# Optimization experiments

Measured on AMD Instinct MI355X. Metric: run time of the kernel, lower is better.

The kernel has to match this reference:

```python
import jax, jax.numpy as jnp
import numpy as np

NEG_SLOPE = 0.2  # PyG GATConv default negative_slope
EPS = 1e-16


def gat_conv(x, W, att_src, att_dst, bias, src, dst, heads, out_ch, concat):
    """PyG-style GATConv (eval mode, self-loops already included in src/dst).
    x: [N, F_in]; W: [heads*out_ch, F_in]; att_src/att_dst: [1, heads, out_ch]; bias: [heads*out_ch] or [out_ch].
    """
    N = x.shape[0]
    h = (x @ W.T).reshape(N, heads, out_ch)            # [N, H, C]
    a_src = (h * att_src).sum(-1)                      # [N, H]
    a_dst = (h * att_dst).sum(-1)                      # [N, H]
    alpha = jax.nn.leaky_relu(a_src[src] + a_dst[dst], NEG_SLOPE)  # [E, H]
    # segment softmax over destination nodes
    amax = jax.ops.segment_max(alpha, dst, num_segments=N)         # [N, H]
    ex = jnp.exp(alpha - amax[dst])
    denom = jax.ops.segment_sum(ex, dst, num_segments=N)           # [N, H]
    coef = ex / (denom[dst] + EPS)                                 # [E, H]
    out = jax.ops.segment_sum(h[src] * coef[:, :, None], dst, num_segments=N)  # [N, H, C]
    if concat:
        out = out.reshape(N, heads * out_ch)
    else:
        out = out.mean(axis=1)
    return out + bias


def setup_inputs() -> dict:
    key = jax.random.key(0)
    ks = jax.random.split(key, 10)
    N, F_in, H, C, OUT, E = 50000, 128, 4, 64, 2, 800000
    x = jax.random.normal(ks[0], (N, F_in), dtype=jnp.float32)
    edge_index = jax.random.randint(ks[1], (2, E), 0, N, dtype=jnp.int64)
    glorot = lambda k, shp: jax.random.normal(k, shp, dtype=jnp.float32) * jnp.sqrt(2.0 / (shp[0] + shp[-1]))
    W1 = glorot(ks[2], (H * C, F_in))
    att_src1 = glorot(ks[3], (1, H, C))
    att_dst1 = glorot(ks[4], (1, H, C))
    b1 = jnp.zeros((H * C,), dtype=jnp.float32)
    W2 = glorot(ks[5], (1 * OUT, H * C))
    att_src2 = glorot(ks[6], (1, 1, OUT))
    att_dst2 = glorot(ks[7], (1, 1, OUT))
    b2 = jnp.zeros((OUT,), dtype=jnp.float32)
    return {"x": x, "edge_index": edge_index, "W1": W1, "att_src1": att_src1,
            "att_dst1": att_dst1, "b1": b1, "W2": W2, "att_src2": att_src2,
            "att_dst2": att_dst2, "b2": b2}


def reference(x, edge_index, W1, att_src1, att_dst1, b1, W2, att_src2, att_dst2, b2):
    N = x.shape[0]
    loop = jnp.arange(N, dtype=edge_index.dtype)
    src = jnp.concatenate([edge_index[0], loop])   # add self-loops (PyG default)
    dst = jnp.concatenate([edge_index[1], loop])
    h = gat_conv(x, W1, att_src1, att_dst1, b1, src, dst, heads=4, out_ch=64, concat=True)
    h = jax.nn.relu(h)
    out = gat_conv(h, W2, att_src2, att_dst2, b2, src, dst, heads=1, out_ch=2, concat=False)
    return out
```

## Files before the change

kernel.cpp:

```cpp
#include <hip/hip_runtime.h>
#include <hip/hip_bf16.h>
#include <stdint.h>

#define NEG_SLOPE 0.2f
#define EPSV 1e-16f
#define SLOT 64
#define NBQ 128
#define NBUCKET 391
#define CAPA 32
#define EPB 8192
#define OVCAP 64

typedef __attribute__((ext_vector_type(8))) short bf16x8;
typedef __attribute__((ext_vector_type(4))) float f32x4;

static __device__ __forceinline__ float b2f(unsigned short u) {
    union { float f; uint32_t i; } v; v.i = ((uint32_t)u) << 16; return v.f;
}
static __device__ __forceinline__ uint32_t qpk(float a, float b) {
    union { float f; uint32_t u; } x, y; x.f = a; y.f = b;
    return ((x.u + 0x8000u) >> 16) | ((y.u + 0x8000u) & 0xFFFF0000u);
}

static __device__ __forceinline__ float edge_exp(float as, float ad) {
    float a = as + ad;
    a = a > 0.f ? a : NEG_SLOPE * a;
    return __expf(a);
}

__global__ __launch_bounds__(256) void fused_front_kernel(
    const float* __restrict__ x, const float* __restrict__ W1,
    const float* __restrict__ att_src1, const float* __restrict__ att_dst1,
    const float* __restrict__ b1, const float* __restrict__ W2,
    const int* __restrict__ ei, int E,
    unsigned short* __restrict__ h1,
    float4* __restrict__ a_src1v, float4* __restrict__ a_dst1v,
    unsigned int* __restrict__ bins, unsigned short* __restrict__ counts,
    unsigned int* __restrict__ gov, unsigned int* __restrict__ govcnt,
    float* __restrict__ b1p, float* __restrict__ w2p0, float* __restrict__ w2p1,
    int N, int nblk_gemm, int nblk_binA)
{
    const int b = blockIdx.x, t = threadIdx.x;

    if (b < nblk_gemm) {
        const int wv = t >> 6, lane = t & 63;
        const int l15 = lane & 15, quad = lane >> 4;
        const int m0 = b * 128 + wv * 32;

        union { bf16x8 v; uint32_t u[4]; } A[2][4];
        #pragma unroll
        for (int ms = 0; ms < 2; ++ms) {
            int m = m0 + ms * 16 + l15;
            int mr = m < N ? m : N - 1;
            const float* ap = x + (size_t)mr * 128 + quad * 8;
            #pragma unroll
            for (int kk = 0; kk < 4; ++kk) {
                float4 u0 = *(const float4*)(ap + kk * 32);
                float4 u1 = *(const float4*)(ap + kk * 32 + 4);
                A[ms][kk].u[0] = qpk(u0.x, u0.y);
                A[ms][kk].u[1] = qpk(u0.z, u0.w);
                A[ms][kk].u[2] = qpk(u1.x, u1.y);
                A[ms][kk].u[3] = qpk(u1.z, u1.w);
            }
        }

        f32x4 acc[2][16];
        #pragma unroll
        for (int ms = 0; ms < 2; ++ms)
            #pragma unroll
            for (int ct = 0; ct < 16; ++ct)
                acc[ms][ct] = (f32x4){0.f, 0.f, 0.f, 0.f};

        #pragma unroll
        for (int kk = 0; kk < 4; ++kk) {
            const float* bpr = W1 + (size_t)l15 * 128 + kk * 32 + quad * 8;
            bf16x8 B[16];
            #pragma unroll
            for (int ct = 0; ct < 16; ++ct) {
                const float* bp = bpr + (size_t)ct * 16 * 128;
                float4 u0 = *(const float4*)(bp);
                float4 u1 = *(const float4*)(bp + 4);
                union { bf16x8 v; uint32_t u[4]; } Bv;
                Bv.u[0] = qpk(u0.x, u0.y);
                Bv.u[1] = qpk(u0.z, u0.w);
                Bv.u[2] = qpk(u1.x, u1.y);
                Bv.u[3] = qpk(u1.z, u1.w);
                B[ct] = Bv.v;
            }
            #pragma unroll
            for (int ct = 0; ct < 16; ++ct) {
                acc[0][ct] = __builtin_amdgcn_mfma_f32_16x16x32_bf16(A[0][kk].v, B[ct], acc[0][ct], 0, 0, 0);
                acc[1][ct] = __builtin_amdgcn_mfma_f32_16x16x32_bf16(A[1][kk].v, B[ct], acc[1][ct], 0, 0, 0);
            }
        }

        #pragma unroll
        for (int ms = 0; ms < 2; ++ms) {
            #pragma unroll
            for (int r = 0; r < 4; ++r) {
                int m = m0 + ms * 16 + quad * 4 + r;
                if (m < N) {
                    uint32_t u[8];
                    #pragma unroll
                    for (int j = 0; j < 8; ++j)
                        u[j] = qpk(acc[ms][2 * j][r], acc[ms][2 * j + 1][r]);
                    uint4* hp = (uint4*)(h1 + (size_t)m * 256 + l15 * 16);
                    hp[0] = make_uint4(u[0], u[1], u[2], u[3]);
                    hp[1] = make_uint4(u[4], u[5], u[6], u[7]);
                }
            }
        }

        float as_l[16], ad_l[16];
        #pragma unroll
        for (int ct = 0; ct < 16; ++ct) {
            as_l[ct] = att_src1[ct * 16 + l15];
            ad_l[ct] = att_dst1[ct * 16 + l15];
        }
        #pragma unroll
        for (int ms = 0; ms < 2; ++ms) {
            #pragma unroll
            for (int r = 0; r < 4; ++r) {
                float ps[4] = {0.f, 0.f, 0.f, 0.f};
                float pd[4] = {0.f, 0.f, 0.f, 0.f};
                #pragma unroll
                for (int ct = 0; ct < 16; ++ct) {
                    ps[ct >> 2] += acc[ms][ct][r] * as_l[ct];
                    pd[ct >> 2] += acc[ms][ct][r] * ad_l[ct];
                }
                #pragma unroll
                for (int off = 1; off < 16; off <<= 1) {
                    #pragma unroll
                    for (int hh = 0; hh < 4; ++hh) {
                        ps[hh] += __shfl_xor(ps[hh], off);
                        pd[hh] += __shfl_xor(pd[hh], off);
                    }
                }
                int m = m0 + ms * 16 + quad * 4 + r;
                if (l15 == 0 && m < N) {
                    a_src1v[m] = make_float4(ps[0], ps[1], ps[2], ps[3]);
                    a_dst1v[m] = make_float4(pd[0], pd[1], pd[2], pd[3]);
                }
            }
        }
    } else if (b < nblk_gemm + nblk_binA) {
        __shared__ unsigned int binS[NBUCKET * CAPA];
        __shared__ unsigned int binC[NBUCKET];
        __shared__ unsigned int ovn;
        const int blk = b - nblk_gemm;

        for (int i = t; i < NBUCKET; i += 256) binC[i] = 0;
        if (t == 0) ovn = 0;
        __syncthreads();

        const int e_base = blk * EPB;
        for (int i = 0; i < EPB / 256; ++i) {
            int e = e_base + i * 256 + t;
            if (e < E) {
                int s = ei[e], d = ei[E + e];
                int bk = d >> 7;
                unsigned int w = (unsigned int)s | ((unsigned int)(d & 127) << 16)
                               | ((unsigned int)bk << 23);
                unsigned int r = atomicAdd(&binC[bk], 1u);
                if (r < CAPA) binS[bk * CAPA + r] = w;
                else {
                    unsigned int o = atomicAdd(&ovn, 1u);
                    if (o < OVCAP) gov[blk * OVCAP + o] = w;
                }
            }
        }
        __syncthreads();

        for (int wdx = t; wdx < NBUCKET * CAPA; wdx += 256) {
            int bk = wdx >> 5, sl = wdx & 31;
            bins[((size_t)bk * nblk_binA + blk) * CAPA + sl] = binS[wdx];
        }
        for (int i = t; i < NBUCKET; i += 256) {
            unsigned int c = binC[i];
            counts[(size_t)i * nblk_binA + blk] = (unsigned short)(c < CAPA ? c : CAPA);
        }
        if (t == 0) govcnt[blk] = (ovn < OVCAP ? ovn : OVCAP);
    } else {
        int cp = t;
        int c = (cp & 15) * 16 + (cp >> 4);
        b1p[cp]  = b1[c];
        w2p0[cp] = W2[c];
        w2p1[cp] = W2[256 + c];
    }
}

__global__ __launch_bounds__(256) void csr_build_kernel(
    const unsigned int* __restrict__ bins, const unsigned short* __restrict__ counts,
    const unsigned int* __restrict__ gov, const unsigned int* __restrict__ govcnt,
    int* __restrict__ deg, unsigned short* __restrict__ csr16,
    int N, int nblk_binA)
{
    const int b = blockIdx.x, t = threadIdx.x;
    const int base = b * NBQ;
    __shared__ unsigned short lcsr[NBQ * SLOT];
    __shared__ unsigned int ldeg[NBQ];

    for (int i = t; i < NBQ; i += 256) {
        ldeg[i] = 1;
        lcsr[i << 6] = (unsigned short)(base + i);
    }
    __syncthreads();

    if (t < 2 * nblk_binA) {
        int cell = t >> 1;
        int c = counts[(size_t)b * nblk_binA + cell];
        const unsigned int* cp = bins + ((size_t)b * nblk_binA + cell) * CAPA;
        for (int r = (t & 1); r < c; r += 2) {
            unsigned int w = cp[r];
            int dl = (w >> 16) & 127;
            unsigned int rank = atomicAdd(&ldeg[dl], 1u);
            if (rank < SLOT) lcsr[(dl << 6) + rank] = (unsigned short)(w & 0xFFFF);
        }
    }
    for (int idx = t; idx < nblk_binA * OVCAP; idx += 256) {
        int blk = idx >> 6, sl = idx & (OVCAP - 1);
        if (sl < (int)govcnt[blk]) {
            unsigned int w = gov[idx];
            if ((int)(w >> 23) == b) {
                int dl = (w >> 16) & 127;
                unsigned int rank = atomicAdd(&ldeg[dl], 1u);
                if (rank < SLOT) lcsr[(dl << 6) + rank] = (unsigned short)(w & 0xFFFF);
            }
        }
    }
    __syncthreads();

    const int nn = min(NBQ, N - base);
    uint4* dst = (uint4*)(csr16 + (size_t)base * SLOT);
    const uint4* src = (const uint4*)lcsr;
    for (int i = t; i < nn * 8; i += 256) dst[i] = src[i];
    for (int i = t; i < nn; i += 256) deg[base + i] = (int)ldeg[i];
}

__global__ __launch_bounds__(256) void agg1_layer2_kernel(
    const int* __restrict__ deg, const unsigned short* __restrict__ csr16,
    const float* __restrict__ a_src1, const float* __restrict__ a_dst1,
    const unsigned short* __restrict__ h1,
    const float* __restrict__ b1p,
    const float* __restrict__ w2p0, const float* __restrict__ w2p1,
    const float* __restrict__ as2, const float* __restrict__ ad2,
    float4* __restrict__ h2pk, int N)
{
    const int wv = threadIdx.x >> 6, lane = threadIdx.x & 63;
    const int half = lane >> 5, ll = lane & 31;
    const int n = blockIdx.x * 4 + wv;
    if (n >= N) return;
    const int h0 = (ll & 1) * 2;
    const unsigned short* cs = csr16 + (size_t)n * SLOT;
    const int dn = deg[n];
    const float2 adh = *(const float2*)(a_dst1 + (size_t)n * 4 + h0);

    float acc[8] = {0.f, 0.f, 0.f, 0.f, 0.f, 0.f, 0.f, 0.f};
    float den0 = 0.f, den1 = 0.f;

    int i = half;
    int s0 = (i < dn) ? (int)cs[i] : -1;
    int s1 = (i + 2 < dn) ? (int)cs[i + 2] : -1;
    float2 as0 = make_float2(0.f, 0.f);
    uint4 r0 = make_uint4(0, 0, 0, 0);
    if (s0 >= 0) {
        as0 = *(const float2*)(a_src1 + (size_t)s0 * 4 + h0);
        r0 = *(const uint4*)(h1 + (size_t)s0 * 256 + ll * 8);
    }
    while (s0 >= 0) {
        int s2 = (i + 4 < dn) ? (int)cs[i + 4] : -1;
        float2 as1 = make_float2(0.f, 0.f);
        uint4 r1 = make_uint4(0, 0, 0, 0);
        if (s1 >= 0) {
            as1 = *(const float2*)(a_src1 + (size_t)s1 * 4 + h0);
            r1 = *(const uint4*)(h1 + (size_t)s1 * 256 + ll * 8);
        }
        float e0 = edge_exp(as0.x, adh.x);
        float e1 = edge_exp(as0.y, adh.y);
        den0 += e0; den1 += e1;
        acc[0] += e0 * b2f((unsigned short)(r0.x & 0xFFFF));
        acc[1] += e0 * b2f((unsigned short)(r0.x >> 16));
        acc[2] += e0 * b2f((unsigned short)(r0.y & 0xFFFF));
        acc[3] += e0 * b2f((unsigned short)(r0.y >> 16));
        acc[4] += e1 * b2f((unsigned short)(r0.z & 0xFFFF));
        acc[5] += e1 * b2f((unsigned short)(r0.z >> 16));
        acc[6] += e1 * b2f((unsigned short)(r0.w & 0xFFFF));
        acc[7] += e1 * b2f((unsigned short)(r0.w >> 16));
        s0 = s1; as0 = as1; r0 = r1; s1 = s2; i += 2;
    }

    #pragma unroll
    for (int k = 0; k < 8; ++k) acc[k] += __shfl_xor(acc[k], 32);
    den0 += __shfl_xor(den0, 32);
    den1 += __shfl_xor(den1, 32);

    const float inv0 = 1.f / (den0 + EPSV);
    const float inv1 = 1.f / (den1 + EPSV);
    const int c0 = ll * 8;
    float4 ba = *(const float4*)(b1p + c0);
    float4 bb = *(const float4*)(b1p + c0 + 4);
    float v[8];
    v[0] = acc[0] * inv0 + ba.x; v[1] = acc[1] * inv0 + ba.y;
    v[2] = acc[2] * inv0 + ba.z; v[3] = acc[3] * inv0 + ba.w;
    v[4] = acc[4] * inv1 + bb.x; v[5] = acc[5] * inv1 + bb.y;
    v[6] = acc[6] * inv1 + bb.z; v[7] = acc[7] * inv1 + bb.w;
    #pragma unroll
    for (int k = 0; k < 8; ++k) v[k] = v[k] > 0.f ? v[k] : 0.f;

    float4 w0a = *(const float4*)(w2p0 + c0);
    float4 w0b = *(const float4*)(w2p0 + c0 + 4);
    float4 w1a = *(const float4*)(w2p1 + c0);
    float4 w1b = *(const float4*)(w2p1 + c0 + 4);
    float p0 = v[0]*w0a.x + v[1]*w0a.y + v[2]*w0a.z + v[3]*w0a.w
             + v[4]*w0b.x + v[5]*w0b.y + v[6]*w0b.z + v[7]*w0b.w;
    float p1 = v[0]*w1a.x + v[1]*w1a.y + v[2]*w1a.z + v[3]*w1a.w
             + v[4]*w1b.x + v[5]*w1b.y + v[6]*w1b.z + v[7]*w1b.w;
    #pragma unroll
    for (int off = 16; off; off >>= 1) {
        p0 += __shfl_xor(p0, off);
        p1 += __shfl_xor(p1, off);
    }
    if (lane == 0) {
        h2pk[n] = make_float4(p0, p1,
                              p0 * as2[0] + p1 * as2[1],
                              p0 * ad2[0] + p1 * ad2[1]);
    }
}

__global__ __launch_bounds__(256) void aggregate2_csr_kernel(
    const int* __restrict__ deg, const unsigned short* __restrict__ csr16,
    const float4* __restrict__ h2pk,
    const float* __restrict__ b2, float* __restrict__ out, int N)
{
    const int wv = threadIdx.x >> 6, lane = threadIdx.x & 63;
    const int g = lane >> 4, q = lane & 15;
    const int n = blockIdx.x * 16 + wv * 4 + g;
    if (n >= N) return;
    const unsigned short* cs = csr16 + (size_t)n * SLOT;
    const int dn = deg[n];
    float ad = h2pk[n].w;
    float den = 0.f, num0 = 0.f, num1 = 0.f;
    for (int i = q; i < dn; i += 16) {
        int s = (int)cs[i];
        float4 hq = h2pk[s];
        float ex = edge_exp(hq.z, ad);
        den  += ex;
        num0 += ex * hq.x;
        num1 += ex * hq.y;
    }
    #pragma unroll
    for (int off = 8; off; off >>= 1) {
        den  += __shfl_xor(den, off);
        num0 += __shfl_xor(num0, off);
        num1 += __shfl_xor(num1, off);
    }
    if (q == 0) {
        float inv = 1.f / (den + EPSV);
        out[(size_t)n * 2]     = num0 * inv + b2[0];
        out[(size_t)n * 2 + 1] = num1 * inv + b2[1];
    }
}

extern "C" void kernel_launch(void* const* d_in, const int* in_sizes, int n_in,
                              void* d_out, int out_size, void* d_ws, size_t ws_size,
                              hipStream_t stream)
{
    const float* x   = (const float*)d_in[0];
    const int*   ei  = (const int*)d_in[1];
    const float* W1  = (const float*)d_in[2];
    const float* as1 = (const float*)d_in[3];
    const float* ad1 = (const float*)d_in[4];
    const float* b1  = (const float*)d_in[5];
    const float* W2  = (const float*)d_in[6];
    const float* as2 = (const float*)d_in[7];
    const float* ad2 = (const float*)d_in[8];
    const float* b2p = (const float*)d_in[9];

    const int N  = in_sizes[0] / 128;
    const int E  = in_sizes[1] / 2;

    const int NB        = (N + NBQ - 1) / NBQ;
    const int nblk_gemm = (N + 127) / 128;
    const int nblk_binA = (E + EPB - 1) / EPB;

    char* ws = (char*)d_ws;
    size_t off = 0;
    auto alloc = [&](size_t bytes) -> char* {
        char* p = ws + off;
        off = (off + bytes + 255) & ~(size_t)255;
        return p;
    };
    unsigned short* h1 = (unsigned short*)alloc((size_t)N * 256 * 2);
    float* a_src1  = (float*)alloc((size_t)N * 4 * 4);
    float* a_dst1  = (float*)alloc((size_t)N * 4 * 4);
    float4* h2pk   = (float4*)alloc((size_t)N * 16);
    float* b1pp    = (float*)alloc((size_t)256 * 4);
    float* w2p0    = (float*)alloc((size_t)256 * 4);
    float* w2p1    = (float*)alloc((size_t)256 * 4);
    int*   deg     = (int*)alloc((size_t)N * 4);
    unsigned short* csr16 = (unsigned short*)alloc((size_t)N * SLOT * 2);
    unsigned int*   bins  = (unsigned int*)alloc((size_t)NB * nblk_binA * CAPA * 4);
    unsigned short* cnts  = (unsigned short*)alloc((size_t)NB * nblk_binA * 2);
    unsigned int*   gov   = (unsigned int*)alloc((size_t)nblk_binA * OVCAP * 4);
    unsigned int*   govcnt= (unsigned int*)alloc((size_t)nblk_binA * 4);

    fused_front_kernel<<<nblk_gemm + nblk_binA + 1, 256, 0, stream>>>(
        x, W1, as1, ad1, b1, W2, ei, E,
        h1, (float4*)a_src1, (float4*)a_dst1,
        bins, cnts, gov, govcnt, b1pp, w2p0, w2p1, N, nblk_gemm, nblk_binA);
    csr_build_kernel<<<NB, 256, 0, stream>>>(
        bins, cnts, gov, govcnt, deg, csr16, N, nblk_binA);
    agg1_layer2_kernel<<<(N + 3) / 4, 256, 0, stream>>>(
        deg, csr16, a_src1, a_dst1, h1,
        b1pp, w2p0, w2p1, as2, ad2, h2pk, N);
    aggregate2_csr_kernel<<<(N + 15) / 16, 256, 0, stream>>>(
        deg, csr16, h2pk, b2p, (float*)d_out, N);
}
```

Baseline: 214.0 us.

## Split GEMM from edge binning and pre-pack W1 to bf16 MFMA layout

The fused front kernel is split in two. One kernel does edge binning and also packs W1 into a bf16 MFMA-fragment layout. A separate GEMM kernel then handles 16 rows per wave instead of 32 and launches with occupancy hint 3. The GEMM now loads pre-converted bf16 B fragments instead of reading fp32 W1 and converting it in every wave. This lowers register pressure and conversion work, at the cost of an extra launch and no longer overlapping the GEMM with binning.

Measured after the change: 203.8 us. -4.8%, faster.

```diff
diff --git a/kernel.cpp b/kernel.cpp
--- a/kernel.cpp
+++ b/kernel.cpp
@@ -10,6 +10,7 @@
 #define CAPA 32
 #define EPB 8192
 #define OVCAP 64
+#define NW1C 16
 
 typedef __attribute__((ext_vector_type(8))) short bf16x8;
 typedef __attribute__((ext_vector_type(4))) float f32x4;
@@ -28,126 +29,23 @@
     return __expf(a);
 }
 
-__global__ __launch_bounds__(256) void fused_front_kernel(
-    const float* __restrict__ x, const float* __restrict__ W1,
-    const float* __restrict__ att_src1, const float* __restrict__ att_dst1,
+__global__ __launch_bounds__(256) void prep_bin_kernel(
+    const int* __restrict__ ei, int E,
+    const float* __restrict__ W1,
     const float* __restrict__ b1, const float* __restrict__ W2,
-    const int* __restrict__ ei, int E,
-    unsigned short* __restrict__ h1,
-    float4* __restrict__ a_src1v, float4* __restrict__ a_dst1v,
     unsigned int* __restrict__ bins, unsigned short* __restrict__ counts,
     unsigned int* __restrict__ gov, unsigned int* __restrict__ govcnt,
+    unsigned short* __restrict__ w1p,
     float* __restrict__ b1p, float* __restrict__ w2p0, float* __restrict__ w2p1,
-    int N, int nblk_gemm, int nblk_binA)
+    int nblk_binA)
 {
     const int b = blockIdx.x, t = threadIdx.x;
 
-    if (b < nblk_gemm) {
-        const int wv = t >> 6, lane = t & 63;
-        const int l15 = lane & 15, quad = lane >> 4;
-        const int m0 = b * 128 + wv * 32;
-
-        union { bf16x8 v; uint32_t u[4]; } A[2][4];
-        #pragma unroll
-        for (int ms = 0; ms < 2; ++ms) {
-            int m = m0 + ms * 16 + l15;
-            int mr = m < N ? m : N - 1;
-            const float* ap = x + (size_t)mr * 128 + quad * 8;
-            #pragma unroll
-            for (int kk = 0; kk < 4; ++kk) {
-                float4 u0 = *(const float4*)(ap + kk * 32);
-                float4 u1 = *(const float4*)(ap + kk * 32 + 4);
-                A[ms][kk].u[0] = qpk(u0.x, u0.y);
-                A[ms][kk].u[1] = qpk(u0.z, u0.w);
-                A[ms][kk].u[2] = qpk(u1.x, u1.y);
-                A[ms][kk].u[3] = qpk(u1.z, u1.w);
-            }
-        }
-
-        f32x4 acc[2][16];
-        #pragma unroll
-        for (int ms = 0; ms < 2; ++ms)
-            #pragma unroll
-            for (int ct = 0; ct < 16; ++ct)
-                acc[ms][ct] = (f32x4){0.f, 0.f, 0.f, 0.f};
-
-        #pragma unroll
-        for (int kk = 0; kk < 4; ++kk) {
-            const float* bpr = W1 + (size_t)l15 * 128 + kk * 32 + quad * 8;
-            bf16x8 B[16];
-            #pragma unroll
-            for (int ct = 0; ct < 16; ++ct) {
-                const float* bp = bpr + (size_t)ct * 16 * 128;
-                float4 u0 = *(const float4*)(bp);
-                float4 u1 = *(const float4*)(bp + 4);
-                union { bf16x8 v; uint32_t u[4]; } Bv;
-                Bv.u[0] = qpk(u0.x, u0.y);
-                Bv.u[1] = qpk(u0.z, u0.w);
-                Bv.u[2] = qpk(u1.x, u1.y);
-                Bv.u[3] = qpk(u1.z, u1.w);
-                B[ct] = Bv.v;
-            }
-            #pragma unroll
-            for (int ct = 0; ct < 16; ++ct) {
-                acc[0][ct] = __builtin_amdgcn_mfma_f32_16x16x32_bf16(A[0][kk].v, B[ct], acc[0][ct], 0, 0, 0);
-                acc[1][ct] = __builtin_amdgcn_mfma_f32_16x16x32_bf16(A[1][kk].v, B[ct], acc[1][ct], 0, 0, 0);
-            }
-        }
-
-        #pragma unroll
-        for (int ms = 0; ms < 2; ++ms) {
-            #pragma unroll
-            for (int r = 0; r < 4; ++r) {
-                int m = m0 + ms * 16 + quad * 4 + r;
-                if (m < N) {
-                    uint32_t u[8];
-                    #pragma unroll
-                    for (int j = 0; j < 8; ++j)
-                        u[j] = qpk(acc[ms][2 * j][r], acc[ms][2 * j + 1][r]);
-                    uint4* hp = (uint4*)(h1 + (size_t)m * 256 + l15 * 16);
-                    hp[0] = make_uint4(u[0], u[1], u[2], u[3]);
-                    hp[1] = make_uint4(u[4], u[5], u[6], u[7]);
-                }
-            }
-        }
-
-        float as_l[16], ad_l[16];
-        #pragma unroll
-        for (int ct = 0; ct < 16; ++ct) {
-            as_l[ct] = att_src1[ct * 16 + l15];
-            ad_l[ct] = att_dst1[ct * 16 + l15];
-        }
-        #pragma unroll
-        for (int ms = 0; ms < 2; ++ms) {
-            #pragma unroll
-            for (int r = 0; r < 4; ++r) {
-                float ps[4] = {0.f, 0.f, 0.f, 0.f};
-                float pd[4] = {0.f, 0.f, 0.f, 0.f};
-                #pragma unroll
-                for (int ct = 0; ct < 16; ++ct) {
-                    ps[ct >> 2] += acc[ms][ct][r] * as_l[ct];
-                    pd[ct >> 2] += acc[ms][ct][r] * ad_l[ct];
-                }
-                #pragma unroll
-                for (int off = 1; off < 16; off <<= 1) {
-                    #pragma unroll
-                    for (int hh = 0; hh < 4; ++hh) {
-                        ps[hh] += __shfl_xor(ps[hh], off);
-                        pd[hh] += __shfl_xor(pd[hh], off);
-                    }
-                }
-                int m = m0 + ms * 16 + quad * 4 + r;
-                if (l15 == 0 && m < N) {
-                    a_src1v[m] = make_float4(ps[0], ps[1], ps[2], ps[3]);
-                    a_dst1v[m] = make_float4(pd[0], pd[1], pd[2], pd[3]);
-                }
-            }
-        }
-    } else if (b < nblk_gemm + nblk_binA) {
+    if (b < nblk_binA) {
         __shared__ unsigned int binS[NBUCKET * CAPA];
         __shared__ unsigned int binC[NBUCKET];
         __shared__ unsigned int ovn;
-        const int blk = b - nblk_gemm;
+        const int blk = b;
 
         for (int i = t; i < NBUCKET; i += 256) binC[i] = 0;
         if (t == 0) ovn = 0;
@@ -180,12 +78,112 @@
             counts[(size_t)i * nblk_binA + blk] = (unsigned short)(c < CAPA ? c : CAPA);
         }
         if (t == 0) govcnt[blk] = (ovn < OVCAP ? ovn : OVCAP);
+    } else if (b < nblk_binA + NW1C) {
+        int idx = (b - nblk_binA) * 256 + t;
+        int c = idx >> 4, oct = idx & 15;
+        int ct = c >> 4, l15 = c & 15;
+        int kk = oct >> 2, quad = oct & 3;
+        const float* sp = W1 + (size_t)c * 128 + oct * 8;
+        float4 u0 = *(const float4*)(sp);
+        float4 u1 = *(const float4*)(sp + 4);
+        uint4 w;
+        w.x = qpk(u0.x, u0.y); w.y = qpk(u0.z, u0.w);
+        w.z = qpk(u1.x, u1.y); w.w = qpk(u1.z, u1.w);
+        *(uint4*)(w1p + (size_t)(((kk * 16 + ct) * 4 + quad) * 128 + l15 * 8)) = w;
     } else {
         int cp = t;
         int c = (cp & 15) * 16 + (cp >> 4);
         b1p[cp]  = b1[c];
         w2p0[cp] = W2[c];
         w2p1[cp] = W2[256 + c];
+    }
+}
+
+__global__ __launch_bounds__(256, 3) void gemm_front_kernel(
+    const float* __restrict__ x,
+    const unsigned short* __restrict__ w1p,
+    const float* __restrict__ att_src1, const float* __restrict__ att_dst1,
+    unsigned short* __restrict__ h1,
+    float4* __restrict__ a_src1v, float4* __restrict__ a_dst1v,
+    int N)
+{
+    const int t = threadIdx.x;
+    const int wv = t >> 6, lane = t & 63;
+    const int l15 = lane & 15, quad = lane >> 4;
+    const int m0 = blockIdx.x * 64 + wv * 16;
+
+    union { bf16x8 v; uint32_t u[4]; } A[4];
+    {
+        int m = m0 + l15;
+        int mr = m < N ? m : N - 1;
+        const float* ap = x + (size_t)mr * 128 + quad * 8;
+        #pragma unroll
+        for (int kk = 0; kk < 4; ++kk) {
+            float4 u0 = *(const float4*)(ap + kk * 32);
+            float4 u1 = *(const float4*)(ap + kk * 32 + 4);
+            A[kk].u[0] = qpk(u0.x, u0.y);
+            A[kk].u[1] = qpk(u0.z, u0.w);
+            A[kk].u[2] = qpk(u1.x, u1.y);
+            A[kk].u[3] = qpk(u1.z, u1.w);
+        }
+    }
+
+    f32x4 acc[16];
+    #pragma unroll
+    for (int ct = 0; ct < 16; ++ct) acc[ct] = (f32x4){0.f, 0.f, 0.f, 0.f};
+
+    const size_t bbase = (size_t)quad * 128 + l15 * 8;
+    #pragma unroll
+    for (int kk = 0; kk < 4; ++kk) {
+        #pragma unroll
+        for (int ct = 0; ct < 16; ++ct) {
+            bf16x8 Bv = *(const bf16x8*)(w1p + (size_t)(kk * 16 + ct) * 512 + bbase);
+            acc[ct] = __builtin_amdgcn_mfma_f32_16x16x32_bf16(A[kk].v, Bv, acc[ct], 0, 0, 0);
+        }
+    }
+
+    #pragma unroll
+    for (int r = 0; r < 4; ++r) {
+        int m = m0 + quad * 4 + r;
+        if (m < N) {
+            uint32_t u[8];
+            #pragma unroll
+            for (int j = 0; j < 8; ++j)
+                u[j] = qpk(acc[2 * j][r], acc[2 * j + 1][r]);
+            uint4* hp = (uint4*)(h1 + (size_t)m * 256 + l15 * 16);
+            hp[0] = make_uint4(u[0], u[1], u[2], u[3]);
+            hp[1] = make_uint4(u[4], u[5], u[6], u[7]);
+        }
+    }
+
+    float as_l[16], ad_l[16];
+    #pragma unroll
+    for (int ct = 0; ct < 16; ++ct) {
+        as_l[ct] = att_src1[ct * 16 + l15];
+        ad_l[ct] = att_dst1[ct * 16 + l15];
+    }
+    #pragma unroll
+    for (int r = 0; r < 4; ++r) {
+        float ps[4] = {0.f, 0.f, 0.f, 0.f};
+        float pd[4] = {0.f, 0.f, 0.f, 0.f};
+        #pragma unroll
+        for (int ct = 0; ct < 16; ++ct) {
+            ps[ct >> 2] += acc[ct][r] * as_l[ct];
+            pd[ct >> 2] += acc[ct][r] * ad_l[ct];
+        }
+        #pragma unroll
+        for (int off = 1; off < 16; off <<= 1) {
+            #pragma unroll
+            for (int hh = 0; hh < 4; ++hh) {
+                ps[hh] += __shfl_xor(ps[hh], off);
+                pd[hh] += __shfl_xor(pd[hh], off);
+            }
+        }
+        int m = m0 + quad * 4 + r;
+        if (l15 == 0 && m < N) {
+            a_src1v[m] = make_float4(ps[0], ps[1], ps[2], ps[3]);
+            a_dst1v[m] = make_float4(pd[0], pd[1], pd[2], pd[3]);
+        }
     }
 }
 
@@ -380,7 +378,6 @@
     const int E  = in_sizes[1] / 2;
 
     const int NB        = (N + NBQ - 1) / NBQ;
-    const int nblk_gemm = (N + 127) / 128;
     const int nblk_binA = (E + EPB - 1) / EPB;
 
     char* ws = (char*)d_ws;
@@ -403,11 +400,13 @@
     unsigned short* cnts  = (unsigned short*)alloc((size_t)NB * nblk_binA * 2);
     unsigned int*   gov   = (unsigned int*)alloc((size_t)nblk_binA * OVCAP * 4);
     unsigned int*   govcnt= (unsigned int*)alloc((size_t)nblk_binA * 4);
-
-    fused_front_kernel<<<nblk_gemm + nblk_binA + 1, 256, 0, stream>>>(
-        x, W1, as1, ad1, b1, W2, ei, E,
-        h1, (float4*)a_src1, (float4*)a_dst1,
-        bins, cnts, gov, govcnt, b1pp, w2p0, w2p1, N, nblk_gemm, nblk_binA);
+    unsigned short* w1pb  = (unsigned short*)alloc((size_t)256 * 128 * 2);
+
+    prep_bin_kernel<<<nblk_binA + NW1C + 1, 256, 0, stream>>>(
+        ei, E, W1, b1, W2,
+        bins, cnts, gov, govcnt, w1pb, b1pp, w2p0, w2p1, nblk_binA);
+    gemm_front_kernel<<<(N + 63) / 64, 256, 0, stream>>>(
+        x, w1pb, as1, ad1, h1, (float4*)a_src1, (float4*)a_dst1, N);
     csr_build_kernel<<<NB, 256, 0, stream>>>(
         bins, cnts, gov, govcnt, deg, csr16, N, nblk_binA);
     agg1_layer2_kernel<<<(N + 3) / 4, 256, 0, stream>>>(
```
